# Kernel tuning notes

Hardware: AMD Instinct MI355X
Metric: run time of the kernel (lower is better)

## Reference

```python
import jax, jax.numpy as jnp
import numpy as np

B, S, D = 2, 2048, 1024
H = 8
HD = D // H  # 128
RANK = 4
CONTROL_SCALE = 1.0


def setup_inputs() -> dict:
    key = jax.random.key(0)
    ks = jax.random.split(key, 8)
    sd = 0.02
    return {
        "hidden_states": jax.random.normal(ks[0], (B, S, D), jnp.float32),
        "control_states": jax.random.normal(ks[1], (B, S, D), jnp.float32),
        "Wq": jax.random.normal(ks[2], (D, D), jnp.float32) * sd,
        "Wk": jax.random.normal(ks[3], (D, D), jnp.float32) * sd,
        "Wv": jax.random.normal(ks[4], (D, D), jnp.float32) * sd,
        "Wo": jax.random.normal(ks[5], (D, D), jnp.float32) * sd,
        "bo": jnp.zeros((D,), jnp.float32),
        "lora_down": jax.random.normal(ks[6], (RANK, D), jnp.float32) * sd,
        "lora_up": jax.random.normal(ks[7], (D, RANK), jnp.float32) * sd,
    }


def _split_heads(x):  # [B,S,D] -> [B,H,S,HD]
    return x.reshape(B, S, H, HD).transpose(0, 2, 1, 3)


def reference(hidden_states, control_states, Wq, Wk, Wv, Wo, bo, lora_down, lora_up):
    # q/k/v projections (Linear, no bias); self-attention (encoder_hidden_states=None)
    q = _split_heads(jnp.einsum("bsd,ed->bse", hidden_states, Wq))
    k = _split_heads(jnp.einsum("bsd,ed->bse", hidden_states, Wk))
    v = _split_heads(jnp.einsum("bsd,ed->bse", hidden_states, Wv))
    inv_sqrt_d = 1.0 / jnp.sqrt(jnp.asarray(HD, q.dtype))
    scores = jnp.einsum("bhqd,bhkd->bhqk", q, k) * inv_sqrt_d  # [B,H,S,S]
    probs = jax.nn.softmax(scores, axis=-1)
    attn_out = jnp.einsum("bhqk,bhkd->bhqd", probs, v)  # [B,H,S,HD]
    attn_out = attn_out.transpose(0, 2, 1, 3).reshape(B, S, D)
    # to_out[0] Linear with bias; to_out[1] Dropout is identity at eval
    out = jnp.einsum("bsd,ed->bse", attn_out, Wo) + bo
    # LoRA control injection: up(down(control_states))
    ctrl = jnp.einsum("bsr,er->bse", jnp.einsum("bsd,rd->bsr", control_states, lora_down), lora_up)
    return out + CONTROL_SCALE * ctrl
```

## Files before the change

kernel.cpp:

```cpp
#include <hip/hip_runtime.h>
#include <hip/hip_bf16.h>


typedef __bf16 bf8_t __attribute__((ext_vector_type(8)));
typedef float f32x4 __attribute__((ext_vector_type(4)));
typedef float f32x16 __attribute__((ext_vector_type(16)));
typedef unsigned u32x4 __attribute__((ext_vector_type(4)));

#define MFMA16(a, b, c) __builtin_amdgcn_mfma_f32_16x16x32_bf16((a), (b), (c), 0, 0, 0)
#define MFMA32(a, b, c) __builtin_amdgcn_mfma_f32_32x32x16_bf16((a), (b), (c), 0, 0, 0)

__device__ __forceinline__ void gload_lds16(const void* g, void* l) {
  __builtin_amdgcn_global_load_lds(
      (const __attribute__((address_space(1))) void*)g,
      (__attribute__((address_space(3))) void*)l, 16, 0, 0);
}

__device__ __forceinline__ unsigned pk2(float a, float b) {
  unsigned short ua = __builtin_bit_cast(unsigned short, (__bf16)a);
  unsigned short ub = __builtin_bit_cast(unsigned short, (__bf16)b);
  return (unsigned)ua | ((unsigned)ub << 16);
}

__global__ __launch_bounds__(256) void cvt5_k(
    const float* __restrict__ s0, const float* __restrict__ s1,
    const float* __restrict__ s2, const float* __restrict__ s3,
    const float* __restrict__ s4, __bf16* __restrict__ d0,
    __bf16* __restrict__ d1, __bf16* __restrict__ d2, __bf16* __restrict__ d3,
    __bf16* __restrict__ d4) {
  const int which = blockIdx.y;
  const float* s = (which == 0) ? s0 : (which == 1) ? s1 : (which == 2) ? s2
                   : (which == 3) ? s3 : s4;
  __bf16* d = (which == 0) ? d0 : (which == 1) ? d1 : (which == 2) ? d2
              : (which == 3) ? d3 : d4;
  const int n = (which == 0) ? (4096 * 1024) : (1024 * 1024);
  const int i = (blockIdx.x * 256 + threadIdx.x) * 8;
  if (i >= n) return;
  float4 a = *(const float4*)(s + i);
  float4 b = *(const float4*)(s + i + 4);
  bf8_t r;
  r[0] = (__bf16)a.x; r[1] = (__bf16)a.y; r[2] = (__bf16)a.z; r[3] = (__bf16)a.w;
  r[4] = (__bf16)b.x; r[5] = (__bf16)b.y; r[6] = (__bf16)b.z; r[7] = (__bf16)b.w;
  *(bf8_t*)(d + i) = r;
}

template <int MR>
__device__ __forceinline__ void gemm_tile(const __bf16* __restrict__ Abase,
                                          const __bf16* __restrict__ Wbase,
                                          int K, __bf16* sA, __bf16* sB,
                                          f32x4 acc[MR][4]) {
  const int tid = threadIdx.x;
  const int wave = tid >> 6, lane = tid & 63;
  const int wr = (wave >> 1) * (MR * 16), wc = (wave & 1) * 64;
  const int lrow = lane >> 3, lchunk = lane & 7;

  for (int m = 0; m < MR; ++m)
    for (int n = 0; n < 4; ++n)
      acc[m][n] = f32x4{0.f, 0.f, 0.f, 0.f};

  for (int k0 = 0; k0 < K; k0 += 64) {
    for (int i = 0; i < MR; ++i) {
      const int rbase = i * 32 + wave * 8;
      gload_lds16(Abase + (size_t)(rbase + lrow) * K + k0 + lchunk * 8,
                  sA + rbase * 64);
    }
    for (int i = 0; i < 4; ++i) {
      const int rbase = i * 32 + wave * 8;
      gload_lds16(Wbase + (size_t)(rbase + lrow) * K + k0 + lchunk * 8,
                  sB + rbase * 64);
    }
    __syncthreads();

    for (int kk = 0; kk < 2; ++kk) {
      bf8_t af[MR], bfr[4];
      const int koff = kk * 32 + (lane >> 4) * 8;
      for (int m = 0; m < MR; ++m)
        af[m] = *(const bf8_t*)&sA[(wr + m * 16 + (lane & 15)) * 64 + koff];
      for (int n = 0; n < 4; ++n)
        bfr[n] = *(const bf8_t*)&sB[(wc + n * 16 + (lane & 15)) * 64 + koff];
      for (int m = 0; m < MR; ++m)
        for (int n = 0; n < 4; ++n)
          acc[m][n] = MFMA16(af[m], bfr[n], acc[m][n]);
    }
    __syncthreads();
  }
}

__global__ __launch_bounds__(256) void gemm_qkv_k(
    const __bf16* __restrict__ X, const __bf16* __restrict__ Wq,
    const __bf16* __restrict__ Wk, const __bf16* __restrict__ Wv,
    __bf16* __restrict__ Qb, __bf16* __restrict__ Kb, __bf16* __restrict__ Vtb) {
  __shared__ __bf16 sA[128 * 64];
  __shared__ __bf16 sB[128 * 64];
  const int z = blockIdx.z;
  const int K = 1024;
  int rowT, colT, Nout;
  const __bf16 *Abase, *Wbase;
  __bf16* C;
  if (z == 2) {
    rowT = blockIdx.x; colT = blockIdx.y; Nout = 4096;
    Abase = Wv + (size_t)rowT * 128 * K;
    Wbase = X + (size_t)colT * 128 * K;
    C = Vtb;
  } else {
    rowT = blockIdx.y; colT = blockIdx.x; Nout = 1024;
    Abase = X + (size_t)rowT * 128 * K;
    Wbase = ((z == 0) ? Wq : Wk) + (size_t)colT * 128 * K;
    C = (z == 0) ? Qb : Kb;
  }
  f32x4 acc[4][4];
  gemm_tile<4>(Abase, Wbase, K, sA, sB, acc);

  const int lane = threadIdx.x & 63, wave = threadIdx.x >> 6;
  const int wr = (wave >> 1) * 64, wc = (wave & 1) * 64;
  const int row0 = rowT * 128 + wr + (lane >> 4) * 4;
  const int col0 = colT * 128 + wc + (lane & 15);
  for (int m = 0; m < 4; ++m)
    for (int n = 0; n < 4; ++n)
      for (int j = 0; j < 4; ++j)
        C[(size_t)(row0 + m * 16 + j) * Nout + col0 + n * 16] = (__bf16)acc[m][n][j];
}

__global__ __launch_bounds__(256) void lora_down_k(
    const float* __restrict__ ctrl, const float* __restrict__ down,
    float* __restrict__ tmp) {
  const int tid = threadIdx.x, wave = tid >> 6, lane = tid & 63;
  const int s = blockIdx.x * 4 + wave;
  const float* cp = ctrl + (size_t)s * 1024 + lane * 16;
  float4 c[4];
  for (int i = 0; i < 4; ++i) c[i] = *(const float4*)(cp + i * 4);
  for (int r = 0; r < 4; ++r) {
    const float* dp = down + r * 1024 + lane * 16;
    float acc = 0.f;
    for (int i = 0; i < 4; ++i) {
      float4 dv = *(const float4*)(dp + i * 4);
      acc += c[i].x * dv.x + c[i].y * dv.y + c[i].z * dv.z + c[i].w * dv.w;
    }
    for (int off = 32; off > 0; off >>= 1) acc += __shfl_xor(acc, off);
    if (lane == 0) tmp[s * 4 + r] = acc;
  }
}

__global__ __launch_bounds__(128) void flash_attn_k(
    const __bf16* __restrict__ Qg, const __bf16* __restrict__ Kg,
    const __bf16* __restrict__ Vtg, __bf16* __restrict__ Op,
    float* __restrict__ ml) {
  const int S = 2048, D = 1024;
  __shared__ __bf16 sK[2][32 * 128];
  __shared__ __bf16 sVt[2][128 * 32];
  __shared__ float sW[2][32];
  const int qt = blockIdx.x, bh = blockIdx.y, z = blockIdx.z;
  const int b = bh >> 3, h = bh & 7;
  const int tid = threadIdx.x, wave = tid >> 6, lane = tid & 63;
  const int l31 = lane & 31, hi = lane >> 5;
  const size_t base = (size_t)b * S * D + (size_t)h * 128;
  const size_t vtbase = (size_t)h * 128 * 4096 + (size_t)b * 2048;
  const int q0 = qt * 64 + wave * 32;
  const int kvbase = z * 1024;

  bf8_t qf[8];
  {
    const float c = 0.08838834764831845f * 1.4426950408889634f;
    const __bf16* qp = Qg + base + (size_t)(q0 + l31) * D + hi * 8;
#pragma unroll
    for (int dc = 0; dc < 8; ++dc) {
      bf8_t v = *(const bf8_t*)(qp + dc * 16);
#pragma unroll
      for (int j = 0; j < 8; ++j) v[j] = (__bf16)((float)v[j] * c);
      qf[dc] = v;
    }
  }

  f32x16 accO[4];
#pragma unroll
  for (int db = 0; db < 4; ++db)
#pragma unroll
    for (int j = 0; j < 16; ++j) accO[db][j] = 0.f;
  float m_ = -1e30f, l_ = 0.f;

  const int krow = wave * 16 + (lane >> 4);
  const __bf16* kgp = Kg + base + (size_t)(kvbase + krow) * D;
  __bf16* klds = &sK[0][0] + (wave * 16) * 128;
  const int vrow = wave * 64 + (lane >> 2);
  const int vgc = ((lane & 3) ^ ((lane >> 3) & 3)) * 8;
  const __bf16* vgp = Vtg + vtbase + (size_t)vrow * 4096 + kvbase + vgc;
  __bf16* vlds = &sVt[0][0] + (wave * 64) * 32;

  auto stageK = [&](int buf, int kv) {
    const __bf16* g = kgp + (size_t)kv * D;
    __bf16* l = klds + buf * (32 * 128);
#pragma unroll
    for (int i = 0; i < 4; ++i) {
      const int gc = (lane & 15) ^ (((lane >> 4) + i * 4) & 7);
      gload_lds16(g + (size_t)(i * 4) * D + gc * 8, l + i * 4 * 128);
    }
  };
  auto stageV = [&](int buf, int kv) {
    const __bf16* g = vgp + kv;
    __bf16* l = vlds + buf * (128 * 32);
#pragma unroll
    for (int i = 0; i < 4; ++i)
      gload_lds16(g + (size_t)(i * 16) * 4096, l + i * 16 * 32);
  };

  stageK(0, 0);
  stageV(0, 0);

  for (int t = 0; t < 32; ++t) {
    const int cur = t & 1;
    __syncthreads();
    if (t < 31) {
      stageK(cur ^ 1, (t + 1) * 32);
      stageV(cur ^ 1, (t + 1) * 32);
    }

    f32x16 accS;
#pragma unroll
    for (int j = 0; j < 16; ++j) accS[j] = 0.f;
    const __bf16* kb_ = sK[cur];
    const int kr = l31;
    __builtin_amdgcn_s_setprio(1);
#pragma unroll
    for (int dc = 0; dc < 8; ++dc) {
      bf8_t a = *(const bf8_t*)&kb_[kr * 128 + ((2 * dc + hi) ^ (kr & 7)) * 8];
      accS = MFMA32(a, qf[dc], accS);
    }
    __builtin_amdgcn_s_setprio(0);

    float pm = fmaxf(accS[0], accS[1]);
#pragma unroll
    for (int j = 2; j < 16; ++j) pm = fmaxf(pm, accS[j]);
    pm = fmaxf(pm, __shfl_xor(pm, 32));

    if (__ballot(pm > m_ + 8.0f)) {
      const float mn = fmaxf(m_, pm);
      const float sc = exp2f(m_ - mn);
      m_ = mn;
      l_ *= sc;
      if (hi == 0) sW[wave][l31] = sc;
#pragma unroll
      for (int r = 0; r < 16; ++r) {
        const float scr = sW[wave][(r & 3) + 8 * (r >> 2) + 4 * hi];
#pragma unroll
        for (int db = 0; db < 4; ++db) accO[db][r] *= scr;
      }
    }

    float rs = 0.f;
#pragma unroll
    for (int j = 0; j < 16; ++j) {
      const float p = exp2f(accS[j] - m_);
      accS[j] = p;
      rs += p;
    }
    rs += __shfl_xor(rs, 32);
    l_ += rs;

    unsigned pk[4][2];
#pragma unroll
    for (int tq = 0; tq < 4; ++tq) {
      pk[tq][0] = pk2(accS[4 * tq + 0], accS[4 * tq + 1]);
      pk[tq][1] = pk2(accS[4 * tq + 2], accS[4 * tq + 3]);
    }

    const __bf16* vt_ = sVt[cur];
#pragma unroll
    for (int kc = 0; kc < 2; ++kc) {
      const unsigned own0 = hi ? pk[2 * kc + 1][0] : pk[2 * kc][0];
      const unsigned own1 = hi ? pk[2 * kc + 1][1] : pk[2 * kc][1];
      const unsigned snd0 = hi ? pk[2 * kc][0] : pk[2 * kc + 1][0];
      const unsigned snd1 = hi ? pk[2 * kc][1] : pk[2 * kc + 1][1];
      const unsigned rc0 = (unsigned)__shfl_xor((int)snd0, 32);
      const unsigned rc1 = (unsigned)__shfl_xor((int)snd1, 32);
      u32x4 fr;
      fr[0] = hi ? rc0 : own0;
      fr[1] = hi ? rc1 : own1;
      fr[2] = hi ? own0 : rc0;
      fr[3] = hi ? own1 : rc1;
      const bf8_t pa = __builtin_bit_cast(bf8_t, fr);
      __builtin_amdgcn_s_setprio(1);
#pragma unroll
      for (int db = 0; db < 4; ++db) {
        const int dr = db * 32 + l31;
        const int p = (kc * 2 + hi) ^ ((dr >> 1) & 3);
        bf8_t vb = *(const bf8_t*)&vt_[dr * 32 + p * 8];
        accO[db] = MFMA32(pa, vb, accO[db]);
      }
      __builtin_amdgcn_s_setprio(0);
    }
  }

  const size_t pbase = ((size_t)(z * 16 + bh) * 2048 + q0);
#pragma unroll
  for (int r = 0; r < 16; ++r) {
    const int qr = (r & 3) + 8 * (r >> 2) + 4 * hi;
    __bf16* op = Op + (pbase + qr) * 128 + l31;
#pragma unroll
    for (int db = 0; db < 4; ++db)
      op[db * 32] = (__bf16)(accO[db][r]);
  }
  if (hi == 0) {
    ml[(pbase + l31) * 2 + 0] = m_;
    ml[(pbase + l31) * 2 + 1] = l_;
  }
}

__global__ __launch_bounds__(256) void attn_merge_k(
    const __bf16* __restrict__ Op, const float* __restrict__ ml,
    __bf16* __restrict__ Og) {
  const int bh = blockIdx.x >> 7, qc = blockIdx.x & 127;
  const int t = threadIdx.x;
  const int qr = qc * 16 + (t >> 4);
  const int d0 = (t & 15) * 8;
  const int b = bh >> 3, h = bh & 7;

  const size_t i0 = ((size_t)bh * 2048 + qr);
  const size_t i1 = ((size_t)(16 + bh) * 2048 + qr);
  const float m0 = ml[i0 * 2], l0 = ml[i0 * 2 + 1];
  const float m1 = ml[i1 * 2], l1 = ml[i1 * 2 + 1];
  const float m = fmaxf(m0, m1);
  const float w0 = exp2f(m0 - m), w1 = exp2f(m1 - m);
  const float inv = 1.0f / (l0 * w0 + l1 * w1);

  bf8_t o0 = *(const bf8_t*)(Op + i0 * 128 + d0);
  bf8_t o1 = *(const bf8_t*)(Op + i1 * 128 + d0);
  bf8_t r;
#pragma unroll
  for (int j = 0; j < 8; ++j)
    r[j] = (__bf16)(((float)o0[j] * w0 + (float)o1[j] * w1) * inv);
  *(bf8_t*)(Og + ((size_t)(b * 2048 + qr) * 1024) + h * 128 + d0) = r;
}

__global__ __launch_bounds__(256) void gemm_out_k(
    const __bf16* __restrict__ A, const __bf16* __restrict__ Wo,
    const float* __restrict__ bo, const float* __restrict__ lup,
    const float* __restrict__ tmp, float* __restrict__ out) {
  __shared__ __bf16 sA[64 * 64];
  __shared__ __bf16 sB[128 * 64];
  const int bcol = blockIdx.x, brow = blockIdx.y;
  const int K = 1024, N = 1024;
  f32x4 acc[2][4];
  gemm_tile<2>(A + (size_t)brow * 64 * K, Wo + (size_t)bcol * 128 * K, K, sA, sB, acc);

  const int lane = threadIdx.x & 63, wave = threadIdx.x >> 6;
  const int wr = (wave >> 1) * 32, wc = (wave & 1) * 64;
  for (int n = 0; n < 4; ++n) {
    const int col = bcol * 128 + wc + n * 16 + (lane & 15);
    const float bias = bo[col];
    const float u0 = lup[col * 4 + 0], u1 = lup[col * 4 + 1];
    const float u2 = lup[col * 4 + 2], u3 = lup[col * 4 + 3];
    for (int m = 0; m < 2; ++m)
      for (int j = 0; j < 4; ++j) {
        const int row = brow * 64 + wr + m * 16 + (lane >> 4) * 4 + j;
        const float* t = tmp + row * 4;
        float v = acc[m][n][j] + bias + t[0] * u0 + t[1] * u1 + t[2] * u2 + t[3] * u3;
        out[(size_t)row * N + col] = v;
      }
  }
}

extern "C" void kernel_launch(void* const* d_in, const int* in_sizes, int n_in,
                              void* d_out, int out_size, void* d_ws, size_t ws_size,
                              hipStream_t stream) {
  (void)in_sizes; (void)n_in; (void)out_size; (void)ws_size;
  const float* hs  = (const float*)d_in[0];
  const float* cs  = (const float*)d_in[1];
  const float* Wq  = (const float*)d_in[2];
  const float* Wk  = (const float*)d_in[3];
  const float* Wv  = (const float*)d_in[4];
  const float* Wo  = (const float*)d_in[5];
  const float* bo  = (const float*)d_in[6];
  const float* ldw = (const float*)d_in[7];
  const float* lup = (const float*)d_in[8];
  float* out = (float*)d_out;

  const size_t MD = (size_t)4096 * 1024;
  const size_t WD = (size_t)1024 * 1024;
  __bf16* hsb = (__bf16*)d_ws;
  __bf16* Wqb = hsb + MD;
  __bf16* Wkb = Wqb + WD;
  __bf16* Wvb = Wkb + WD;
  __bf16* Wob = Wvb + WD;
  __bf16* Qb  = Wob + WD;
  __bf16* Kb  = Qb + MD;
  __bf16* Vtb = Kb + MD;
  __bf16* Ab  = Vtb + MD;
  float*  tmp = (float*)(Ab + MD);
  __bf16* Opart = (__bf16*)(tmp + 4096 * 4);
  float*  mlp   = (float*)(Opart + (size_t)2 * 16 * 2048 * 128);

  cvt5_k<<<dim3(2048, 5), 256, 0, stream>>>(hs, Wq, Wk, Wv, Wo,
                                            hsb, Wqb, Wkb, Wvb, Wob);
  gemm_qkv_k<<<dim3(8, 32, 3), 256, 0, stream>>>(hsb, Wqb, Wkb, Wvb, Qb, Kb, Vtb);
  lora_down_k<<<dim3(1024), 256, 0, stream>>>(cs, ldw, tmp);
  flash_attn_k<<<dim3(32, 16, 2), 128, 0, stream>>>(Qb, Kb, Vtb, Opart, mlp);
  attn_merge_k<<<dim3(2048), 256, 0, stream>>>(Opart, mlp, Ab);
  gemm_out_k<<<dim3(8, 64), 256, 0, stream>>>(Ab, Wob, bo, lup, tmp, out);
}
```

Baseline: 164.7 us.

## Split attention KV into four chunks and load V directly from global

```diff
diff --git a/kernel.cpp b/kernel.cpp
--- a/kernel.cpp
+++ b/kernel.cpp
@@ -146,8 +146,8 @@
     const __bf16* __restrict__ Vtg, __bf16* __restrict__ Op,
     float* __restrict__ ml) {
   const int S = 2048, D = 1024;
+  const int NT = 16;
   __shared__ __bf16 sK[2][32 * 128];
-  __shared__ __bf16 sVt[2][128 * 32];
   __shared__ float sW[2][32];
   const int qt = blockIdx.x, bh = blockIdx.y, z = blockIdx.z;
   const int b = bh >> 3, h = bh & 7;
@@ -156,7 +156,7 @@
   const size_t base = (size_t)b * S * D + (size_t)h * 128;
   const size_t vtbase = (size_t)h * 128 * 4096 + (size_t)b * 2048;
   const int q0 = qt * 64 + wave * 32;
-  const int kvbase = z * 1024;
+  const int kvofs = z * 512;
 
   bf8_t qf[8];
   {
@@ -179,13 +179,8 @@
   float m_ = -1e30f, l_ = 0.f;
 
   const int krow = wave * 16 + (lane >> 4);
-  const __bf16* kgp = Kg + base + (size_t)(kvbase + krow) * D;
+  const __bf16* kgp = Kg + base + (size_t)(kvofs + krow) * D;
   __bf16* klds = &sK[0][0] + (wave * 16) * 128;
-  const int vrow = wave * 64 + (lane >> 2);
-  const int vgc = ((lane & 3) ^ ((lane >> 3) & 3)) * 8;
-  const __bf16* vgp = Vtg + vtbase + (size_t)vrow * 4096 + kvbase + vgc;
-  __bf16* vlds = &sVt[0][0] + (wave * 64) * 32;
-
   auto stageK = [&](int buf, int kv) {
     const __bf16* g = kgp + (size_t)kv * D;
     __bf16* l = klds + buf * (32 * 128);
@@ -195,24 +190,22 @@
       gload_lds16(g + (size_t)(i * 4) * D + gc * 8, l + i * 4 * 128);
     }
   };
-  auto stageV = [&](int buf, int kv) {
-    const __bf16* g = vgp + kv;
-    __bf16* l = vlds + buf * (128 * 32);
-#pragma unroll
-    for (int i = 0; i < 4; ++i)
-      gload_lds16(g + (size_t)(i * 16) * 4096, l + i * 16 * 32);
-  };
+
+  const __bf16* vg0 = Vtg + vtbase + (size_t)l31 * 4096 + kvofs + hi * 8;
 
   stageK(0, 0);
-  stageV(0, 0);
-
-  for (int t = 0; t < 32; ++t) {
+
+  for (int t = 0; t < NT; ++t) {
     const int cur = t & 1;
     __syncthreads();
-    if (t < 31) {
-      stageK(cur ^ 1, (t + 1) * 32);
-      stageV(cur ^ 1, (t + 1) * 32);
-    }
+    if (t < NT - 1) stageK(cur ^ 1, (t + 1) * 32);
+
+    bf8_t vr[2][4];
+#pragma unroll
+    for (int kc = 0; kc < 2; ++kc)
+#pragma unroll
+      for (int db = 0; db < 4; ++db)
+        vr[kc][db] = *(const bf8_t*)(vg0 + (size_t)(db * 32) * 4096 + t * 32 + kc * 16);
 
     f32x16 accS;
 #pragma unroll
@@ -227,9 +220,12 @@
     }
     __builtin_amdgcn_s_setprio(0);
 
-    float pm = fmaxf(accS[0], accS[1]);
-#pragma unroll
-    for (int j = 2; j < 16; ++j) pm = fmaxf(pm, accS[j]);
+    float mx[8];
+#pragma unroll
+    for (int j = 0; j < 8; ++j) mx[j] = fmaxf(accS[2 * j], accS[2 * j + 1]);
+#pragma unroll
+    for (int j = 0; j < 4; ++j) mx[j] = fmaxf(mx[j], mx[j + 4]);
+    float pm = fmaxf(fmaxf(mx[0], mx[1]), fmaxf(mx[2], mx[3]));
     pm = fmaxf(pm, __shfl_xor(pm, 32));
 
     if (__ballot(pm > m_ + 8.0f)) {
@@ -246,13 +242,18 @@
       }
     }
 
-    float rs = 0.f;
+    float sm[16];
 #pragma unroll
     for (int j = 0; j < 16; ++j) {
       const float p = exp2f(accS[j] - m_);
       accS[j] = p;
-      rs += p;
-    }
+      sm[j] = p;
+    }
+#pragma unroll
+    for (int j = 0; j < 8; ++j) sm[j] += sm[j + 8];
+#pragma unroll
+    for (int j = 0; j < 4; ++j) sm[j] += sm[j + 4];
+    float rs = (sm[0] + sm[1]) + (sm[2] + sm[3]);
     rs += __shfl_xor(rs, 32);
     l_ += rs;
 
@@ -263,7 +264,6 @@
       pk[tq][1] = pk2(accS[4 * tq + 2], accS[4 * tq + 3]);
     }
 
-    const __bf16* vt_ = sVt[cur];
 #pragma unroll
     for (int kc = 0; kc < 2; ++kc) {
       const unsigned own0 = hi ? pk[2 * kc + 1][0] : pk[2 * kc][0];
@@ -280,12 +280,8 @@
       const bf8_t pa = __builtin_bit_cast(bf8_t, fr);
       __builtin_amdgcn_s_setprio(1);
 #pragma unroll
-      for (int db = 0; db < 4; ++db) {
-        const int dr = db * 32 + l31;
-        const int p = (kc * 2 + hi) ^ ((dr >> 1) & 3);
-        bf8_t vb = *(const bf8_t*)&vt_[dr * 32 + p * 8];
-        accO[db] = MFMA32(pa, vb, accO[db]);
-      }
+      for (int db = 0; db < 4; ++db)
+        accO[db] = MFMA32(pa, vr[kc][db], accO[db]);
       __builtin_amdgcn_s_setprio(0);
     }
   }
@@ -314,20 +310,34 @@
   const int d0 = (t & 15) * 8;
   const int b = bh >> 3, h = bh & 7;
 
-  const size_t i0 = ((size_t)bh * 2048 + qr);
-  const size_t i1 = ((size_t)(16 + bh) * 2048 + qr);
-  const float m0 = ml[i0 * 2], l0 = ml[i0 * 2 + 1];
-  const float m1 = ml[i1 * 2], l1 = ml[i1 * 2 + 1];
-  const float m = fmaxf(m0, m1);
-  const float w0 = exp2f(m0 - m), w1 = exp2f(m1 - m);
-  const float inv = 1.0f / (l0 * w0 + l1 * w1);
-
-  bf8_t o0 = *(const bf8_t*)(Op + i0 * 128 + d0);
-  bf8_t o1 = *(const bf8_t*)(Op + i1 * 128 + d0);
+  size_t idx[4];
+  float mi[4], li[4];
+  float m = -1e30f;
+#pragma unroll
+  for (int i = 0; i < 4; ++i) {
+    idx[i] = ((size_t)(i * 16 + bh) * 2048 + qr);
+    mi[i] = ml[idx[i] * 2];
+    li[i] = ml[idx[i] * 2 + 1];
+    m = fmaxf(m, mi[i]);
+  }
+  float den = 0.f, w[4];
+#pragma unroll
+  for (int i = 0; i < 4; ++i) {
+    w[i] = exp2f(mi[i] - m);
+    den += li[i] * w[i];
+  }
+  const float inv = 1.0f / den;
+
+  float acc[8] = {0, 0, 0, 0, 0, 0, 0, 0};
+#pragma unroll
+  for (int i = 0; i < 4; ++i) {
+    bf8_t o = *(const bf8_t*)(Op + idx[i] * 128 + d0);
+#pragma unroll
+    for (int j = 0; j < 8; ++j) acc[j] += (float)o[j] * w[i];
+  }
   bf8_t r;
 #pragma unroll
-  for (int j = 0; j < 8; ++j)
-    r[j] = (__bf16)(((float)o0[j] * w0 + (float)o1[j] * w1) * inv);
+  for (int j = 0; j < 8; ++j) r[j] = (__bf16)(acc[j] * inv);
   *(bf8_t*)(Og + ((size_t)(b * 2048 + qr) * 1024) + h * 128 + d0) = r;
 }
 
@@ -387,13 +397,13 @@
   __bf16* Ab  = Vtb + MD;
   float*  tmp = (float*)(Ab + MD);
   __bf16* Opart = (__bf16*)(tmp + 4096 * 4);
-  float*  mlp   = (float*)(Opart + (size_t)2 * 16 * 2048 * 128);
+  float*  mlp   = (float*)(Opart + (size_t)4 * 16 * 2048 * 128);
 
   cvt5_k<<<dim3(2048, 5), 256, 0, stream>>>(hs, Wq, Wk, Wv, Wo,
                                             hsb, Wqb, Wkb, Wvb, Wob);
   gemm_qkv_k<<<dim3(8, 32, 3), 256, 0, stream>>>(hsb, Wqb, Wkb, Wvb, Qb, Kb, Vtb);
   lora_down_k<<<dim3(1024), 256, 0, stream>>>(cs, ldw, tmp);
-  flash_attn_k<<<dim3(32, 16, 2), 128, 0, stream>>>(Qb, Kb, Vtb, Opart, mlp);
+  flash_attn_k<<<dim3(32, 16, 4), 128, 0, stream>>>(Qb, Kb, Vtb, Opart, mlp);
   attn_merge_k<<<dim3(2048), 256, 0, stream>>>(Opart, mlp, Ab);
   gemm_out_k<<<dim3(8, 64), 256, 0, stream>>>(Ab, Wob, bo, lup, tmp, out);
 }
```

New measurement: 218.6 us. 1.33x slower.

## Split QK MFMA chain, tree-reduce softmax, defer row-sum shuffle, remap block order

Applied to the files above, without the earlier changes.

```diff
diff --git a/kernel.cpp b/kernel.cpp
--- a/kernel.cpp
+++ b/kernel.cpp
@@ -146,17 +146,24 @@
     const __bf16* __restrict__ Vtg, __bf16* __restrict__ Op,
     float* __restrict__ ml) {
   const int S = 2048, D = 1024;
+  const int NT = 16;
   __shared__ __bf16 sK[2][32 * 128];
   __shared__ __bf16 sVt[2][128 * 32];
   __shared__ float sW[2][32];
-  const int qt = blockIdx.x, bh = blockIdx.y, z = blockIdx.z;
+
+  const int lin = blockIdx.x + 32 * (blockIdx.y + 16 * blockIdx.z);
+  const int s7 = lin >> 3;
+  const int bh = (lin & 7) * 2 + (s7 >> 6);
+  const int qt = s7 & 31;
+  const int z = (s7 >> 5) & 1;
+
   const int b = bh >> 3, h = bh & 7;
   const int tid = threadIdx.x, wave = tid >> 6, lane = tid & 63;
   const int l31 = lane & 31, hi = lane >> 5;
   const size_t base = (size_t)b * S * D + (size_t)h * 128;
   const size_t vtbase = (size_t)h * 128 * 4096 + (size_t)b * 2048;
   const int q0 = qt * 64 + wave * 32;
-  const int kvbase = z * 1024;
+  const int kvofs = z * 1024;
 
   bf8_t qf[8];
   {
@@ -179,11 +186,11 @@
   float m_ = -1e30f, l_ = 0.f;
 
   const int krow = wave * 16 + (lane >> 4);
-  const __bf16* kgp = Kg + base + (size_t)(kvbase + krow) * D;
+  const __bf16* kgp = Kg + base + (size_t)(kvofs + krow) * D;
   __bf16* klds = &sK[0][0] + (wave * 16) * 128;
   const int vrow = wave * 64 + (lane >> 2);
   const int vgc = ((lane & 3) ^ ((lane >> 3) & 3)) * 8;
-  const __bf16* vgp = Vtg + vtbase + (size_t)vrow * 4096 + kvbase + vgc;
+  const __bf16* vgp = Vtg + vtbase + (size_t)vrow * 4096 + kvofs + vgc;
   __bf16* vlds = &sVt[0][0] + (wave * 64) * 32;
 
   auto stageK = [&](int buf, int kv) {
@@ -214,22 +221,30 @@
       stageV(cur ^ 1, (t + 1) * 32);
     }
 
-    f32x16 accS;
-#pragma unroll
-    for (int j = 0; j < 16; ++j) accS[j] = 0.f;
+    f32x16 a0, a1;
+#pragma unroll
+    for (int j = 0; j < 16; ++j) { a0[j] = 0.f; a1[j] = 0.f; }
     const __bf16* kb_ = sK[cur];
     const int kr = l31;
     __builtin_amdgcn_s_setprio(1);
 #pragma unroll
-    for (int dc = 0; dc < 8; ++dc) {
-      bf8_t a = *(const bf8_t*)&kb_[kr * 128 + ((2 * dc + hi) ^ (kr & 7)) * 8];
-      accS = MFMA32(a, qf[dc], accS);
+    for (int dc = 0; dc < 4; ++dc) {
+      bf8_t ka = *(const bf8_t*)&kb_[kr * 128 + ((2 * dc + hi) ^ (kr & 7)) * 8];
+      a0 = MFMA32(ka, qf[dc], a0);
+      bf8_t kb2 = *(const bf8_t*)&kb_[kr * 128 + ((2 * (dc + 4) + hi) ^ (kr & 7)) * 8];
+      a1 = MFMA32(kb2, qf[dc + 4], a1);
     }
     __builtin_amdgcn_s_setprio(0);
-
-    float pm = fmaxf(accS[0], accS[1]);
-#pragma unroll
-    for (int j = 2; j < 16; ++j) pm = fmaxf(pm, accS[j]);
+    f32x16 accS;
+#pragma unroll
+    for (int j = 0; j < 16; ++j) accS[j] = a0[j] + a1[j];
+
+    float mx[8];
+#pragma unroll
+    for (int j = 0; j < 8; ++j) mx[j] = fmaxf(accS[2 * j], accS[2 * j + 1]);
+#pragma unroll
+    for (int j = 0; j < 4; ++j) mx[j] = fmaxf(mx[j], mx[j + 4]);
+    float pm = fmaxf(fmaxf(mx[0], mx[1]), fmaxf(mx[2], mx[3]));
     pm = fmaxf(pm, __shfl_xor(pm, 32));
 
     if (__ballot(pm > m_ + 8.0f)) {
@@ -246,15 +261,18 @@
       }
     }
 
-    float rs = 0.f;
+    float sm[16];
 #pragma unroll
     for (int j = 0; j < 16; ++j) {
       const float p = exp2f(accS[j] - m_);
       accS[j] = p;
-      rs += p;
-    }
-    rs += __shfl_xor(rs, 32);
-    l_ += rs;
+      sm[j] = p;
+    }
+#pragma unroll
+    for (int j = 0; j < 8; ++j) sm[j] += sm[j + 8];
+#pragma unroll
+    for (int j = 0; j < 4; ++j) sm[j] += sm[j + 4];
+    l_ += (sm[0] + sm[1]) + (sm[2] + sm[3]);
 
     unsigned pk[4][2];
 #pragma unroll
@@ -290,6 +308,8 @@
     }
   }
 
+  const float lf = l_ + __shfl_xor(l_, 32);
+
   const size_t pbase = ((size_t)(z * 16 + bh) * 2048 + q0);
 #pragma unroll
   for (int r = 0; r < 16; ++r) {
@@ -301,7 +321,7 @@
   }
   if (hi == 0) {
     ml[(pbase + l31) * 2 + 0] = m_;
-    ml[(pbase + l31) * 2 + 1] = l_;
+    ml[(pbase + l31) * 2 + 1] = lf;
   }
 }
 
```

Measured after the change: 199.3 us. +21.0%, slower.
